# Optimization experiments

Hardware: AMD Instinct MI355X
Metric: run time of the kernel (lower is better)

## Reference

```python
import jax, jax.numpy as jnp
import numpy as np

RANK = 8
A_SHAPE = (64, 128)   # (a1, a2)
B_SHAPE = (16, 32)    # (b1, b2)
BATCH = 16384


def setup_inputs() -> dict:
    key = jax.random.key(0)
    k1, k2, k3, k4, k5 = jax.random.split(key, 5)
    a1, a2 = A_SHAPE
    b1, b2 = B_SHAPE
    x = jax.random.normal(k1, (BATCH, a1 * b1), dtype=jnp.float32)
    # xavier-uniform style init for a and b (as in nn.init.xavier_uniform_)
    lim_a = float(np.sqrt(6.0 / (a1 + a2)))
    lim_b = float(np.sqrt(6.0 / (b1 + b2)))
    a = jax.random.uniform(k2, (RANK, a1, a2), minval=-lim_a, maxval=lim_a, dtype=jnp.float32)
    b = jax.random.uniform(k3, (RANK, b1, b2), minval=-lim_b, maxval=lim_b, dtype=jnp.float32)
    s = jax.random.normal(k4, (a1, a2), dtype=jnp.float32)          # structured-sparse mask
    bias = jax.random.normal(k5, (a2 * b2,), dtype=jnp.float32)     # bias_shape[1:] = (a2*b2,)
    return {"x": x, "a": a, "b": b, "s": s, "bias": bias}


def reference(x, a, b, s, bias):
    # structured-sparse elementwise mask on a
    a_eff = s[None, :, :] * a                          # (rank, a1, a2)
    r, a1, a2 = a_eff.shape
    _, b1, b2 = b.shape
    # w = sum_r kron(a_eff[r], b[r]) : (a1*b1, a2*b2)
    w = jnp.einsum('rij,rkl->ikjl', a_eff, b).reshape(a1 * b1, a2 * b2)
    out = x @ w                                        # (batch, a2*b2)
    return out + bias[None, :]
```

## Files before the change

kernel.cpp:

```cpp
#include <hip/hip_runtime.h>
#include <hip/hip_bf16.h>

typedef short bf16x8 __attribute__((ext_vector_type(8)));
typedef float f32x4 __attribute__((ext_vector_type(4)));

static constexpr int M_DIM = 16384;
static constexpr int N_DIM = 4096;
static constexpr int K_DIM = 1024;

static constexpr int CVT_BLOCKS = (M_DIM * K_DIM / 8) / 256;
static constexpr int WT_BLOCKS  = N_DIM;

__device__ __forceinline__ unsigned short f2bf(float f) {
  union { float f; unsigned u; } v; v.f = f;
  unsigned r = v.u + 0x7FFFu + ((v.u >> 16) & 1u);
  return (unsigned short)(r >> 16);
}

__global__ __launch_bounds__(256) void prep_kernel(
    const float* __restrict__ x, const float* __restrict__ a,
    const float* __restrict__ b, const float* __restrict__ s,
    unsigned short* __restrict__ xb, unsigned short* __restrict__ wT) {
  __shared__ float as_eff[8][64];
  __shared__ float bl[8][16];
  const int tid = threadIdx.x;

  if (blockIdx.x < CVT_BLOCKS) {
    const int i = (blockIdx.x * 256 + tid) * 2;
    float4 v0 = reinterpret_cast<const float4*>(x)[i];
    float4 v1 = reinterpret_cast<const float4*>(x)[i + 1];
    ushort4 o0, o1;
    o0.x = f2bf(v0.x); o0.y = f2bf(v0.y); o0.z = f2bf(v0.z); o0.w = f2bf(v0.w);
    o1.x = f2bf(v1.x); o1.y = f2bf(v1.y); o1.z = f2bf(v1.z); o1.w = f2bf(v1.w);
    reinterpret_cast<ushort4*>(xb)[i] = o0;
    reinterpret_cast<ushort4*>(xb)[i + 1] = o1;
    return;
  }

  const int n = blockIdx.x - CVT_BLOCKS;
  const int j = n >> 5, l = n & 31;

#pragma unroll
  for (int t = tid; t < 512; t += 256) {
    const int r = t >> 6, i = t & 63;
    as_eff[r][i] = a[(r * 64 + i) * 128 + j] * s[i * 128 + j];
  }
  if (tid < 128) {
    const int r = tid >> 4, kk = tid & 15;
    bl[r][kk] = b[(r * 16 + kk) * 32 + l];
  }
  __syncthreads();

  const int i = tid >> 2;
  const int kk0 = (tid & 3) * 4;
  float o[4] = {0.f, 0.f, 0.f, 0.f};
#pragma unroll
  for (int r = 0; r < 8; ++r) {
    const float av = as_eff[r][i];
#pragma unroll
    for (int q = 0; q < 4; ++q)
      o[q] += av * bl[r][kk0 + q];
  }
  ushort4 w4;
  w4.x = f2bf(o[0]); w4.y = f2bf(o[1]); w4.z = f2bf(o[2]); w4.w = f2bf(o[3]);
  *reinterpret_cast<ushort4*>(&wT[(size_t)n * K_DIM + tid * 4]) = w4;
}


#define PH_BARRIER __builtin_amdgcn_s_barrier()
#define SCHED0     __builtin_amdgcn_sched_barrier(0)
#define WAITV(N)   do { asm volatile("s_waitcnt vmcnt(" #N ")" ::: "memory"); SCHED0; } while (0)
#define WAITL(N)   do { asm volatile("s_waitcnt lgkmcnt(" #N ")" ::: "memory"); SCHED0; } while (0)

__device__ __forceinline__ void quad_mfma(f32x4 (&acc)[8][4], const bf16x8 (&aH)[4][2],
                                          const bf16x8 (&bH)[2][2], int mbase, int nbase) {
  __builtin_amdgcn_s_setprio(1);
#pragma unroll
  for (int ks = 0; ks < 2; ++ks)
#pragma unroll
    for (int mi = 0; mi < 4; ++mi)
#pragma unroll
      for (int ni = 0; ni < 2; ++ni)
        acc[mbase + mi][nbase + ni] = __builtin_amdgcn_mfma_f32_16x16x32_bf16(
            aH[mi][ks], bH[ni][ks], acc[mbase + mi][nbase + ni], 0, 0, 0);
  __builtin_amdgcn_s_setprio(0);
}

__global__ __launch_bounds__(512, 2) void gemm8_kernel(
    const unsigned short* __restrict__ A, const unsigned short* __restrict__ BT,
    const float* __restrict__ bias, float* __restrict__ C) {
  __shared__ __align__(16) unsigned short Al[2][16384];
  __shared__ __align__(16) unsigned short Bl[2][16384];

  const int tid  = threadIdx.x;
  const int lane = tid & 63;
  const int wave = tid >> 6;
  const int wm = wave >> 2;
  const int wn = wave & 3;
  const int wr = wm * 128;
  const int wc = wn * 64;
  const int frow = lane & 15;
  const int kg = lane >> 4;
  const int swz0 = (kg * 16) ^ ((lane & 7) << 4);
  const int swz1 = (64 + kg * 16) ^ ((lane & 7) << 4);

  int bid = blockIdx.x;
  int gid = bid >> 4, lid = bid & 15;
  gid = ((gid & 7) << 3) | (gid >> 3);
  const int bm = (gid >> 2) * 4 + (lid >> 2);
  const int bn = (gid & 3) * 4 + (lid & 3);
  const int brow = bm * 256, bcol = bn * 256;

  const unsigned short* Abase = A + (size_t)brow * K_DIM;
  const unsigned short* Bbase = BT + (size_t)bcol * K_DIM;

  const int srow = tid >> 3;
  const int scol = ((((tid & 7) << 4) ^ ((srow & 7) << 4)) >> 1);
  const int ldsu = __builtin_amdgcn_readfirstlane(wave * 512);

#define STG(dst, base, q, k0) __builtin_amdgcn_global_load_lds( \
    (const __attribute__((address_space(1))) void*)((base) + (size_t)((q)*64 + srow) * K_DIM + (k0) + scol), \
    (__attribute__((address_space(3))) void*)((dst) + (q)*4096 + ldsu), 16, 0, 0)

#define STG4(dst, base, k0) do { STG(dst, base, 0, k0); STG(dst, base, 1, k0); \
                                 STG(dst, base, 2, k0); STG(dst, base, 3, k0); } while (0)

#define LOAD_AH(P, h, dst) { _Pragma("unroll") for (int mi = 0; mi < 4; ++mi) { \
    const char* p_ = (const char*)(P) + (wr + frow + ((h)*4 + mi) * 16) * 128; \
    dst[mi][0] = *(const bf16x8*)(p_ + swz0); dst[mi][1] = *(const bf16x8*)(p_ + swz1); } }

#define LOAD_BH(P, h, dst) { _Pragma("unroll") for (int ni = 0; ni < 2; ++ni) { \
    const char* p_ = (const char*)(P) + (wc + frow + ((h)*2 + ni) * 16) * 128; \
    dst[ni][0] = *(const bf16x8*)(p_ + swz0); dst[ni][1] = *(const bf16x8*)(p_ + swz1); } }

  f32x4 acc[8][4] = {};
  bf16x8 aF0[4][2], aF1[4][2], b0[2][2], b1[2][2];

  STG4(Bl[0], Bbase, 0);
  STG4(Al[0], Abase, 0);
  STG4(Bl[1], Bbase, 64);
  WAITV(4);
  PH_BARRIER;

#define TILE(PA, PB, SA, SB, VM) \
  LOAD_AH(PA, 0, aF0); SCHED0; \
  LOAD_BH(PB, 0, b0);  SCHED0; \
  LOAD_BH(PB, 1, b1);  SCHED0; \
  LOAD_AH(PA, 1, aF1); SCHED0; \
  SA; \
  WAITL(12); \
  quad_mfma(acc, aF0, b0, 0, 0); \
  WAITL(8); \
  quad_mfma(acc, aF0, b1, 0, 2); \
  WAITL(0); \
  PH_BARRIER; \
  SB; \
  quad_mfma(acc, aF1, b0, 4, 0); \
  quad_mfma(acc, aF1, b1, 4, 2); \
  VM; \
  PH_BARRIER;

  int k = 0;
#pragma unroll 1
  for (int i = 0; i < 7; ++i) {
    TILE(Al[0], Bl[0], STG4(Al[1], Abase, k + 64), STG4(Bl[0], Bbase, k + 128), WAITV(4));
    TILE(Al[1], Bl[1], STG4(Al[0], Abase, k + 128), STG4(Bl[1], Bbase, k + 192), WAITV(4));
    k += 128;
  }
  TILE(Al[0], Bl[0], STG4(Al[1], Abase, k + 64), (void)0, WAITV(0));
  TILE(Al[1], Bl[1], (void)0, (void)0, WAITV(0));

  __syncthreads();
  float* T = (float*)&Al[0][0];
  float* Tw = T + wave * (16 * 68);
  const int col4 = lane & 15;
  const int rsel = lane >> 4;
  float4 bv = *(const float4*)&bias[bcol + wc + col4 * 4];

#pragma unroll
  for (int mi = 0; mi < 8; ++mi) {
#pragma unroll
    for (int ni = 0; ni < 4; ++ni)
#pragma unroll
      for (int r = 0; r < 4; ++r)
        Tw[(kg * 4 + r) * 68 + ni * 16 + frow] = acc[mi][ni][r];
    WAITL(0);
#pragma unroll
    for (int rr = 0; rr < 4; ++rr) {
      float4 v = *(float4*)&Tw[(rr * 4 + rsel) * 68 + col4 * 4];
      v.x += bv.x; v.y += bv.y; v.z += bv.z; v.w += bv.w;
      *(float4*)&C[(size_t)(brow + wr + mi * 16 + rr * 4 + rsel) * N_DIM + bcol + wc + col4 * 4] = v;
    }
    WAITL(0);
  }
}

extern "C" void kernel_launch(void* const* d_in, const int* in_sizes, int n_in,
                              void* d_out, int out_size, void* d_ws, size_t ws_size,
                              hipStream_t stream) {
  const float* x    = (const float*)d_in[0];
  const float* a    = (const float*)d_in[1];
  const float* b    = (const float*)d_in[2];
  const float* s    = (const float*)d_in[3];
  const float* bias = (const float*)d_in[4];
  float* out = (float*)d_out;

  unsigned short* xb = (unsigned short*)d_ws;
  unsigned short* wT = (unsigned short*)((char*)d_ws + (size_t)M_DIM * K_DIM * 2);

  prep_kernel<<<CVT_BLOCKS + WT_BLOCKS, 256, 0, stream>>>(x, a, b, s, xb, wT);
  gemm8_kernel<<<(M_DIM / 256) * (N_DIM / 256), 512, 0, stream>>>(xb, wT, bias, out);
}
```

Measured before the change: 183.7 us.

## Switch GEMM inner loop to 32x32x16 bf16 MFMA with restructured fragment loads

Replaces the 16x16x32 MFMA tiling with 32x32x16 bf16 MFMAs. Each wave now holds 4x2 accumulators of 16 floats instead of 8x4 of 4. The LDS fragment loads and swizzle are rewritten per k-step, interleaved with four MFMA groups per tile, and the epilogue is remapped to the 32x32 output layout. The goal is fewer MFMA issues and fewer LDS fragment reads per FLOP, at the cost of a new wait/overlap schedule and a bank-conflict pattern that may differ.

Measured after the change: 197.0 us. 1.07x slower.

```diff
diff --git a/kernel.cpp b/kernel.cpp
--- a/kernel.cpp
+++ b/kernel.cpp
@@ -2,7 +2,7 @@
 #include <hip/hip_bf16.h>
 
 typedef short bf16x8 __attribute__((ext_vector_type(8)));
-typedef float f32x4 __attribute__((ext_vector_type(4)));
+typedef float f32x16 __attribute__((ext_vector_type(16)));
 
 static constexpr int M_DIM = 16384;
 static constexpr int N_DIM = 4096;
@@ -72,21 +72,7 @@
 #define WAITV(N)   do { asm volatile("s_waitcnt vmcnt(" #N ")" ::: "memory"); SCHED0; } while (0)
 #define WAITL(N)   do { asm volatile("s_waitcnt lgkmcnt(" #N ")" ::: "memory"); SCHED0; } while (0)
 
-__device__ __forceinline__ void quad_mfma(f32x4 (&acc)[8][4], const bf16x8 (&aH)[4][2],
-                                          const bf16x8 (&bH)[2][2], int mbase, int nbase) {
-  __builtin_amdgcn_s_setprio(1);
-#pragma unroll
-  for (int ks = 0; ks < 2; ++ks)
-#pragma unroll
-    for (int mi = 0; mi < 4; ++mi)
-#pragma unroll
-      for (int ni = 0; ni < 2; ++ni)
-        acc[mbase + mi][nbase + ni] = __builtin_amdgcn_mfma_f32_16x16x32_bf16(
-            aH[mi][ks], bH[ni][ks], acc[mbase + mi][nbase + ni], 0, 0, 0);
-  __builtin_amdgcn_s_setprio(0);
-}
-
-__global__ __launch_bounds__(512, 2) void gemm8_kernel(
+__global__ __launch_bounds__(512, 2) void gemm_kernel(
     const unsigned short* __restrict__ A, const unsigned short* __restrict__ BT,
     const float* __restrict__ bias, float* __restrict__ C) {
   __shared__ __align__(16) unsigned short Al[2][16384];
@@ -99,10 +85,9 @@
   const int wn = wave & 3;
   const int wr = wm * 128;
   const int wc = wn * 64;
-  const int frow = lane & 15;
-  const int kg = lane >> 4;
-  const int swz0 = (kg * 16) ^ ((lane & 7) << 4);
-  const int swz1 = (64 + kg * 16) ^ ((lane & 7) << 4);
+  const int r32 = lane & 31;
+  const int hi  = lane >> 5;
+  const int x7  = r32 & 7;
 
   int bid = blockIdx.x;
   int gid = bid >> 4, lid = bid & 15;
@@ -125,16 +110,23 @@
 #define STG4(dst, base, k0) do { STG(dst, base, 0, k0); STG(dst, base, 1, k0); \
                                  STG(dst, base, 2, k0); STG(dst, base, 3, k0); } while (0)
 
-#define LOAD_AH(P, h, dst) { _Pragma("unroll") for (int mi = 0; mi < 4; ++mi) { \
-    const char* p_ = (const char*)(P) + (wr + frow + ((h)*4 + mi) * 16) * 128; \
-    dst[mi][0] = *(const bf16x8*)(p_ + swz0); dst[mi][1] = *(const bf16x8*)(p_ + swz1); } }
-
-#define LOAD_BH(P, h, dst) { _Pragma("unroll") for (int ni = 0; ni < 2; ++ni) { \
-    const char* p_ = (const char*)(P) + (wc + frow + ((h)*2 + ni) * 16) * 128; \
-    dst[ni][0] = *(const bf16x8*)(p_ + swz0); dst[ni][1] = *(const bf16x8*)(p_ + swz1); } }
-
-  f32x4 acc[8][4] = {};
-  bf16x8 aF0[4][2], aF1[4][2], b0[2][2], b1[2][2];
+#define LDKS(PA, PB, ks_) { \
+    const int ch_ = ((((ks_)*2 + hi) ^ x7) << 4); \
+    _Pragma("unroll") for (int mi = 0; mi < 4; ++mi) \
+      aF[mi][ks_] = *(const bf16x8*)((const char*)(PA) + (wr + mi * 32 + r32) * 128 + ch_); \
+    _Pragma("unroll") for (int ni = 0; ni < 2; ++ni) \
+      bF[ni][ks_] = *(const bf16x8*)((const char*)(PB) + (wc + ni * 32 + r32) * 128 + ch_); \
+  }
+
+#define MFMA8(ks_) do { __builtin_amdgcn_s_setprio(1); \
+    _Pragma("unroll") for (int mi = 0; mi < 4; ++mi) \
+    _Pragma("unroll") for (int ni = 0; ni < 2; ++ni) \
+      acc[mi][ni] = __builtin_amdgcn_mfma_f32_32x32x16_bf16( \
+          aF[mi][ks_], bF[ni][ks_], acc[mi][ni], 0, 0, 0); \
+    __builtin_amdgcn_s_setprio(0); } while (0)
+
+  f32x16 acc[4][2] = {};
+  bf16x8 aF[4][4], bF[2][4];
 
   STG4(Bl[0], Bbase, 0);
   STG4(Al[0], Abase, 0);
@@ -143,20 +135,19 @@
   PH_BARRIER;
 
 #define TILE(PA, PB, SA, SB, VM) \
-  LOAD_AH(PA, 0, aF0); SCHED0; \
-  LOAD_BH(PB, 0, b0);  SCHED0; \
-  LOAD_BH(PB, 1, b1);  SCHED0; \
-  LOAD_AH(PA, 1, aF1); SCHED0; \
+  LDKS(PA, PB, 0); LDKS(PA, PB, 1); SCHED0; \
   SA; \
+  WAITL(6); \
+  MFMA8(0); \
+  LDKS(PA, PB, 2); LDKS(PA, PB, 3); SCHED0; \
   WAITL(12); \
-  quad_mfma(acc, aF0, b0, 0, 0); \
-  WAITL(8); \
-  quad_mfma(acc, aF0, b1, 0, 2); \
+  MFMA8(1); \
+  WAITL(6); \
+  MFMA8(2); \
   WAITL(0); \
   PH_BARRIER; \
   SB; \
-  quad_mfma(acc, aF1, b0, 4, 0); \
-  quad_mfma(acc, aF1, b1, 4, 2); \
+  MFMA8(3); \
   VM; \
   PH_BARRIER;
 
@@ -178,20 +169,25 @@
   float4 bv = *(const float4*)&bias[bcol + wc + col4 * 4];
 
 #pragma unroll
-  for (int mi = 0; mi < 8; ++mi) {
-#pragma unroll
-    for (int ni = 0; ni < 4; ++ni)
-#pragma unroll
-      for (int r = 0; r < 4; ++r)
-        Tw[(kg * 4 + r) * 68 + ni * 16 + frow] = acc[mi][ni][r];
-    WAITL(0);
-#pragma unroll
-    for (int rr = 0; rr < 4; ++rr) {
-      float4 v = *(float4*)&Tw[(rr * 4 + rsel) * 68 + col4 * 4];
-      v.x += bv.x; v.y += bv.y; v.z += bv.z; v.w += bv.w;
-      *(float4*)&C[(size_t)(brow + wr + mi * 16 + rr * 4 + rsel) * N_DIM + bcol + wc + col4 * 4] = v;
+  for (int fm = 0; fm < 4; ++fm) {
+#pragma unroll
+    for (int mfh = 0; mfh < 2; ++mfh) {
+#pragma unroll
+      for (int ni = 0; ni < 2; ++ni)
+#pragma unroll
+        for (int qq = 0; qq < 2; ++qq)
+#pragma unroll
+          for (int r = 0; r < 4; ++r)
+            Tw[(qq * 8 + hi * 4 + r) * 68 + ni * 32 + r32] = acc[fm][ni][(2 * mfh + qq) * 4 + r];
+      WAITL(0);
+#pragma unroll
+      for (int rr = 0; rr < 4; ++rr) {
+        float4 v = *(float4*)&Tw[(rr * 4 + rsel) * 68 + col4 * 4];
+        v.x += bv.x; v.y += bv.y; v.z += bv.z; v.w += bv.w;
+        *(float4*)&C[(size_t)(brow + wr + fm * 32 + mfh * 16 + rr * 4 + rsel) * N_DIM + bcol + wc + col4 * 4] = v;
+      }
+      WAITL(0);
     }
-    WAITL(0);
   }
 }
 
@@ -209,5 +205,5 @@
   unsigned short* wT = (unsigned short*)((char*)d_ws + (size_t)M_DIM * K_DIM * 2);
 
   prep_kernel<<<CVT_BLOCKS + WT_BLOCKS, 256, 0, stream>>>(x, a, b, s, xb, wT);
-  gemm8_kernel<<<(M_DIM / 256) * (N_DIM / 256), 512, 0, stream>>>(xb, wT, bias, out);
-}
+  gemm_kernel<<<(M_DIM / 256) * (N_DIM / 256), 512, 0, stream>>>(xb, wT, bias, out);
+}
```
